# Kernel optimization log

Measured on AMD Instinct MI355X. Metric: run time of the kernel, lower is better.

## Reference

```python
import jax, jax.numpy as jnp
import numpy as np

HIDDEN = 64


def _lstm_cell(x, h, c, W_ih, W_hh, b_ih, b_hh):
    # gates: [B, 4*H], torch LSTMCell order: i, f, g, o
    gates = x @ W_ih.T + h @ W_hh.T + b_ih + b_hh
    i, f, g, o = jnp.split(gates, 4, axis=-1)
    i = jax.nn.sigmoid(i)
    f = jax.nn.sigmoid(f)
    g = jnp.tanh(g)
    o = jax.nn.sigmoid(o)
    c_new = f * c + i * g
    h_new = o * jnp.tanh(c_new)
    return h_new, c_new


def setup_inputs() -> dict:
    key = jax.random.key(0)
    ks = jax.random.split(key, 12)
    B, L, H = 1024, 512, HIDDEN
    k = 1.0 / np.sqrt(H)  # torch LSTMCell/Linear init scale
    u = lambda kk, shape: jax.random.uniform(kk, shape, jnp.float32, -k, k)
    return {
        "y": jax.random.normal(ks[0], (B, L), jnp.float32),
        "W_ih1": u(ks[1], (4 * H, 1)),
        "W_hh1": u(ks[2], (4 * H, H)),
        "b_ih1": u(ks[3], (4 * H,)),
        "b_hh1": u(ks[4], (4 * H,)),
        "W_ih2": u(ks[5], (4 * H, H)),
        "W_hh2": u(ks[6], (4 * H, H)),
        "b_ih2": u(ks[7], (4 * H,)),
        "b_hh2": u(ks[8], (4 * H,)),
        "W_lin": u(ks[9], (1, H)),
        "b_lin": u(ks[10], (1,)),
        "future_preds": 0,
    }


def reference(y, W_ih1, W_hh1, b_ih1, b_hh1, W_ih2, W_hh2, b_ih2, b_hh2,
              W_lin, b_lin, future_preds):
    B = y.shape[0]
    H = HIDDEN
    zeros = jnp.zeros((B, H), jnp.float32)

    def step(carry, x_t):
        h1, c1, h2, c2 = carry
        h1, c1 = _lstm_cell(x_t, h1, c1, W_ih1, W_hh1, b_ih1, b_hh1)
        h2, c2 = _lstm_cell(h1, h2, c2, W_ih2, W_hh2, b_ih2, b_hh2)
        out = h2 @ W_lin.T + b_lin  # [B, 1]
        return (h1, c1, h2, c2), out

    xs = y.T[:, :, None]  # [L, B, 1]
    carry, outs = jax.lax.scan(step, (zeros, zeros, zeros, zeros), xs)
    outputs = outs[:, :, 0].T  # [B, L]

    if future_preds > 0:
        def fstep(fc, _):
            h1, c1, h2, c2, out = fc
            h1, c1 = _lstm_cell(out, h1, c1, W_ih1, W_hh1, b_ih1, b_hh1)
            h2, c2 = _lstm_cell(h1, h2, c2, W_ih2, W_hh2, b_ih2, b_hh2)
            out = h2 @ W_lin.T + b_lin
            return (h1, c1, h2, c2, out), out
        last_out = outs[-1]  # [B, 1]
        _, fouts = jax.lax.scan(fstep, (*carry, last_out), None,
                                length=future_preds)
        outputs = jnp.concatenate([outputs, fouts[:, :, 0].T], axis=1)
    return outputs
```

## Files before the change

kernel.cpp:

```cpp
#include <hip/hip_runtime.h>
#include <math.h>

#define LSEQ 512

typedef float  f32x4  __attribute__((ext_vector_type(4)));
typedef short  bf16x8 __attribute__((ext_vector_type(8)));

union Frag { uint32_t u[4]; bf16x8 h; };

__device__ __forceinline__ float frcp(float x) { return __builtin_amdgcn_rcpf(x); }

__device__ __forceinline__ f32x4 vexp2(f32x4 x) {
    f32x4 r;
    r.x = exp2f(x.x); r.y = exp2f(x.y); r.z = exp2f(x.z); r.w = exp2f(x.w);
    return r;
}
__device__ __forceinline__ f32x4 vrcp(f32x4 x) {
    f32x4 r;
    r.x = frcp(x.x); r.y = frcp(x.y); r.z = frcp(x.z); r.w = frcp(x.w);
    return r;
}
__device__ __forceinline__ f32x4 vsigm(f32x4 x) {
    f32x4 e = vexp2(x * -1.442695041f);
    return vrcp(e + 1.0f);
}
__device__ __forceinline__ f32x4 vtanh(f32x4 x) {
    f32x4 e = vexp2(x * 2.885390082f);
    return 1.0f - 2.0f * vrcp(e + 1.0f);
}

__device__ __forceinline__ uint32_t pack_hi_u(uint32_t b0, uint32_t b1) {
    return __builtin_amdgcn_perm(b1, b0, 0x07060302u);
}

__device__ __forceinline__ void load_wfrag(const float* __restrict__ W, int sl, int nn, int g4,
                                           Frag fh[4][2], Frag fl[4][2]) {
#pragma unroll
    for (int gt = 0; gt < 4; ++gt) {
        const float* p = W + (size_t)(64 * gt + 16 * sl + nn) * 64 + g4 * 8;
#pragma unroll
        for (int kt = 0; kt < 2; ++kt) {
            float4 va = ((const float4*)(p + kt * 32))[0];
            float4 vb = ((const float4*)(p + kt * 32))[1];
            float v[8] = {va.x, va.y, va.z, va.w, vb.x, vb.y, vb.z, vb.w};
#pragma unroll
            for (int j = 0; j < 4; ++j) {
                uint32_t b0 = __float_as_uint(v[2 * j]);
                uint32_t b1 = __float_as_uint(v[2 * j + 1]);
                float l0 = v[2 * j]     - __uint_as_float(b0 & 0xffff0000u);
                float l1 = v[2 * j + 1] - __uint_as_float(b1 & 0xffff0000u);
                fh[gt][kt].u[j] = pack_hi_u(b0, b1);
                fl[gt][kt].u[j] = pack_hi_u(__float_as_uint(l0), __float_as_uint(l1));
            }
        }
    }
}

__device__ __forceinline__ int hidx(int m, int j) {
    return m * 64 + ((((j >> 3) ^ (m & 7)) << 3) | (j & 7));
}

__device__ __forceinline__ void loadA(const uint16_t* __restrict__ ph,
                                      const uint16_t* __restrict__ pl,
                                      int mm, int g4, bf16x8 ah[2], bf16x8 al[2]) {
#pragma unroll
    for (int kt = 0; kt < 2; ++kt) {
        const int off = mm * 64 + ((((kt << 2) + g4) ^ (mm & 7)) << 3);
        ah[kt] = *(const bf16x8*)(ph + off);
        al[kt] = *(const bf16x8*)(pl + off);
    }
}

__device__ __forceinline__ void split_store(uint16_t* ph, uint16_t* pl, int idx, float x) {
    uint32_t xb = __float_as_uint(x);
    ph[idx] = (uint16_t)(xb >> 16);
    float lo = x - __uint_as_float(xb & 0xffff0000u);
    pl[idx] = (uint16_t)(__float_as_uint(lo) >> 16);
}

#define MFMA3(acc, AH, AL, BH, BL)                                                  \
    acc = __builtin_amdgcn_mfma_f32_16x16x32_bf16((AH), (BH).h, acc, 0, 0, 0);      \
    acc = __builtin_amdgcn_mfma_f32_16x16x32_bf16((AH), (BL).h, acc, 0, 0, 0);      \
    acc = __builtin_amdgcn_mfma_f32_16x16x32_bf16((AL), (BH).h, acc, 0, 0, 0);

__global__ __launch_bounds__(512, 1)
void lstm2_pipe(const float* __restrict__ y,
                const float* __restrict__ W_ih1, const float* __restrict__ W_hh1,
                const float* __restrict__ b_ih1, const float* __restrict__ b_hh1,
                const float* __restrict__ W_ih2, const float* __restrict__ W_hh2,
                const float* __restrict__ b_ih2, const float* __restrict__ b_hh2,
                const float* __restrict__ W_lin, const float* __restrict__ b_lin,
                float* __restrict__ out)
{
    __shared__ __align__(16) float    y_s[LSEQ * 16];
    __shared__ __align__(16) uint16_t h1h[2][1024];
    __shared__ __align__(16) uint16_t h1l[2][1024];
    __shared__ __align__(16) uint16_t h2h[2][1024];
    __shared__ __align__(16) uint16_t h2l[2][1024];
    __shared__ __align__(16) float    outS[16 * 521];

    const int tid  = threadIdx.x;
    const int w    = tid >> 6;
    const int lane = tid & 63;
    const int nn   = lane & 15;
    const int g4   = lane >> 4;
    const int mq   = g4 << 2;
    const int bg0  = blockIdx.x << 4;

    {
        const int m = tid >> 5, seg = tid & 31;
        const float4* yp = (const float4*)(y + (size_t)(bg0 + m) * LSEQ) + seg * 4;
#pragma unroll
        for (int c = 0; c < 4; ++c) {
            float4 v = yp[c];
            int t0 = seg * 16 + c * 4;
            y_s[(t0 + 0) * 16 + m] = v.x;
            y_s[(t0 + 1) * 16 + m] = v.y;
            y_s[(t0 + 2) * 16 + m] = v.z;
            y_s[(t0 + 3) * 16 + m] = v.w;
        }
        if (tid < 256) {
            uint4 z = {0u, 0u, 0u, 0u};
            ((uint4*)h1h)[tid] = z;
            ((uint4*)h1l)[tid] = z;
            ((uint4*)h2h)[tid] = z;
            ((uint4*)h2l)[tid] = z;
        }
    }
    __syncthreads();

    if (w < 4) {
        Frag bh[4][2], bl[4][2];
        load_wfrag(W_hh1, w, nn, g4, bh, bl);
        float bs1_[4], wih1_[4];
#pragma unroll
        for (int gt = 0; gt < 4; ++gt) {
            int row = 64 * gt + 16 * w + nn;
            bs1_[gt]  = b_ih1[row] + b_hh1[row];
            wih1_[gt] = W_ih1[row];
        }
        const int jj = 16 * w + nn;
        f32x4 c1v = {0.f, 0.f, 0.f, 0.f};

        float wl[16];
        const float blin = b_lin[0];
        {
            const float4* wp = (const float4*)W_lin + g4 * 4;
#pragma unroll
            for (int i = 0; i < 4; ++i) {
                float4 v = wp[i];
                wl[4 * i + 0] = v.x; wl[4 * i + 1] = v.y;
                wl[4 * i + 2] = v.z; wl[4 * i + 3] = v.w;
            }
        }

#pragma unroll 1
        for (int t = 0; t <= LSEQ; ++t) {
            if (t < LSEQ) {
                bf16x8 ah[2], al[2];
                loadA(h1h[(t + 1) & 1], h1l[(t + 1) & 1], nn, g4, ah, al);
                f32x4 xq = *(const f32x4*)&y_s[t * 16 + mq];
                f32x4 ac0[4], ac1[4];
#pragma unroll
                for (int g = 0; g < 4; ++g) {
                    ac0[g] = xq * wih1_[g] + bs1_[g];
                    ac1[g] = 0.f;
                }
#pragma unroll
                for (int g = 0; g < 4; ++g) {
                    MFMA3(ac0[g], ah[0], al[0], bh[g][0], bl[g][0]);
                    MFMA3(ac1[g], ah[1], al[1], bh[g][1], bl[g][1]);
                }
                f32x4 gi = vsigm(ac0[0] + ac1[0]);
                f32x4 gf = vsigm(ac0[1] + ac1[1]);
                f32x4 gg = vtanh(ac0[2] + ac1[2]);
                f32x4 go = vsigm(ac0[3] + ac1[3]);
                c1v = gf * c1v + gi * gg;
                f32x4 h1v = go * vtanh(c1v);
#pragma unroll
                for (int r = 0; r < 4; ++r)
                    split_store(h1h[t & 1], h1l[t & 1], hidx(mq + r, jj), h1v[r]);
            }
            if (t >= 2 && w == ((t - 2) & 3)) {
                const uint16_t* ph = h2h[t & 1];
                const uint16_t* pl = h2l[t & 1];
                const int m = lane & 15;
                float s = 0.f;
#pragma unroll
                for (int oo = 0; oo < 2; ++oo) {
                    const int oct = 2 * g4 + oo;
                    const int off = m * 64 + ((oct ^ (m & 7)) << 3);
                    bf16x8 hv = *(const bf16x8*)(ph + off);
                    bf16x8 lv = *(const bf16x8*)(pl + off);
#pragma unroll
                    for (int i = 0; i < 8; ++i) {
                        float val = __uint_as_float(((uint32_t)(uint16_t)hv[i]) << 16)
                                  + __uint_as_float(((uint32_t)(uint16_t)lv[i]) << 16);
                        s = fmaf(val, wl[oo * 8 + i], s);
                    }
                }
                s += __shfl_xor(s, 16);
                s += __shfl_xor(s, 32);
                if (lane < 16) outS[m * 521 + (t - 2)] = s + blin;
            }
            __syncthreads();
        }
        if (w == 0) {
            const uint16_t* ph = h2h[1];
            const uint16_t* pl = h2l[1];
            const int m = lane & 15;
            float s = 0.f;
#pragma unroll
            for (int oo = 0; oo < 2; ++oo) {
                const int oct = 2 * g4 + oo;
                const int off = m * 64 + ((oct ^ (m & 7)) << 3);
                bf16x8 hv = *(const bf16x8*)(ph + off);
                bf16x8 lv = *(const bf16x8*)(pl + off);
#pragma unroll
                for (int i = 0; i < 8; ++i) {
                    float val = __uint_as_float(((uint32_t)(uint16_t)hv[i]) << 16)
                              + __uint_as_float(((uint32_t)(uint16_t)lv[i]) << 16);
                    s = fmaf(val, wl[oo * 8 + i], s);
                }
            }
            s += __shfl_xor(s, 16);
            s += __shfl_xor(s, 32);
            if (lane < 16) outS[m * 521 + (LSEQ - 1)] = s + blin;
        }
    } else {
        const int v = w - 4;
        Frag bih[4][2], bil[4][2], bhh[4][2], bhl[4][2];
        load_wfrag(W_ih2, v, nn, g4, bih, bil);
        load_wfrag(W_hh2, v, nn, g4, bhh, bhl);
        float bs2_[4];
#pragma unroll
        for (int gt = 0; gt < 4; ++gt) {
            int row = 64 * gt + 16 * v + nn;
            bs2_[gt] = b_ih2[row] + b_hh2[row];
        }
        const int jj = 16 * v + nn;
        f32x4 c2v = {0.f, 0.f, 0.f, 0.f};

#pragma unroll 1
        for (int t = 0; t <= LSEQ; ++t) {
            if (t >= 1) {
                bf16x8 a3h_[2], a3l_[2], a2h_[2], a2l_[2];
                loadA(h2h[t & 1],       h2l[t & 1],       nn, g4, a3h_, a3l_);
                loadA(h1h[(t - 1) & 1], h1l[(t - 1) & 1], nn, g4, a2h_, a2l_);
                f32x4 aca[4], acb[4];
#pragma unroll
                for (int g = 0; g < 4; ++g) { acb[g] = bs2_[g]; aca[g] = 0.f; }
                __builtin_amdgcn_s_setprio(1);
#pragma unroll
                for (int kt = 0; kt < 2; ++kt)
#pragma unroll
                    for (int g = 0; g < 4; ++g) {
                        MFMA3(acb[g], a3h_[kt], a3l_[kt], bhh[g][kt], bhl[g][kt]);
                        MFMA3(aca[g], a2h_[kt], a2l_[kt], bih[g][kt], bil[g][kt]);
                    }
                __builtin_amdgcn_s_setprio(0);
                f32x4 gi = vsigm(aca[0] + acb[0]);
                f32x4 gf = vsigm(aca[1] + acb[1]);
                f32x4 gg = vtanh(aca[2] + acb[2]);
                f32x4 go = vsigm(aca[3] + acb[3]);
                c2v = gf * c2v + gi * gg;
                f32x4 h2v = go * vtanh(c2v);
#pragma unroll
                for (int r = 0; r < 4; ++r)
                    split_store(h2h[(t - 1) & 1], h2l[(t - 1) & 1], hidx(mq + r, jj), h2v[r]);
            }
            __syncthreads();
        }
    }

    __syncthreads();

    {
        const int m  = tid >> 5;
        const int t0 = (tid & 31) << 4;
        float* op = out + (size_t)(bg0 + m) * LSEQ + t0;
        const float* sp = outS + m * 521 + t0;
#pragma unroll
        for (int k2 = 0; k2 < 4; ++k2) {
            float4 vv = make_float4(sp[4 * k2 + 0], sp[4 * k2 + 1],
                                    sp[4 * k2 + 2], sp[4 * k2 + 3]);
            *(float4*)(op + 4 * k2) = vv;
        }
    }
}

extern "C" void kernel_launch(void* const* d_in, const int* in_sizes, int n_in,
                              void* d_out, int out_size, void* d_ws, size_t ws_size,
                              hipStream_t stream) {
    const float* y     = (const float*)d_in[0];
    const float* W_ih1 = (const float*)d_in[1];
    const float* W_hh1 = (const float*)d_in[2];
    const float* b_ih1 = (const float*)d_in[3];
    const float* b_hh1 = (const float*)d_in[4];
    const float* W_ih2 = (const float*)d_in[5];
    const float* W_hh2 = (const float*)d_in[6];
    const float* b_ih2 = (const float*)d_in[7];
    const float* b_hh2 = (const float*)d_in[8];
    const float* W_lin = (const float*)d_in[9];
    const float* b_lin = (const float*)d_in[10];
    float* out = (float*)d_out;

    lstm2_pipe<<<dim3(64), dim3(512), 0, stream>>>(
        y, W_ih1, W_hh1, b_ih1, b_hh1, W_ih2, W_hh2, b_ih2, b_hh2,
        W_lin, b_lin, out);
}
```

Measured before the change: 826.6 us.

## Skew layer-2 input projection one step ahead and compute output head via MFMA

The layer-2 warps now compute the W_ih2·h1 projection one timestep ahead into a register accumulator, so each step's critical path only runs the W_hh2 recurrent MFMAs before the gate math. This lengthens the pipeline by one extra step. The scalar per-lane linear output head, which rotated across warps, is replaced by a single warp issuing MFMAs against a zero-padded W_lin fragment, with the outS layout transposed to match. Layer-1 MFMAs also get raised scheduling priority.

```diff
diff --git a/kernel.cpp b/kernel.cpp
--- a/kernel.cpp
+++ b/kernel.cpp
@@ -97,7 +97,7 @@
     __shared__ __align__(16) uint16_t h1l[2][1024];
     __shared__ __align__(16) uint16_t h2h[2][1024];
     __shared__ __align__(16) uint16_t h2l[2][1024];
-    __shared__ __align__(16) float    outS[16 * 521];
+    __shared__ __align__(16) float    outS[LSEQ * 20];
 
     const int tid  = threadIdx.x;
     const int w    = tid >> 6;
@@ -141,21 +141,33 @@
         }
         const int jj = 16 * w + nn;
         f32x4 c1v = {0.f, 0.f, 0.f, 0.f};
-
-        float wl[16];
         const float blin = b_lin[0];
-        {
-            const float4* wp = (const float4*)W_lin + g4 * 4;
-#pragma unroll
-            for (int i = 0; i < 4; ++i) {
-                float4 v = wp[i];
-                wl[4 * i + 0] = v.x; wl[4 * i + 1] = v.y;
-                wl[4 * i + 2] = v.z; wl[4 * i + 3] = v.w;
+
+        Frag wlh[2], wll[2];
+#pragma unroll
+        for (int kt = 0; kt < 2; ++kt) {
+            if (nn == 0) {
+                const float* p = W_lin + kt * 32 + g4 * 8;
+                float4 va = ((const float4*)p)[0];
+                float4 vb = ((const float4*)p)[1];
+                float vv[8] = {va.x, va.y, va.z, va.w, vb.x, vb.y, vb.z, vb.w};
+#pragma unroll
+                for (int j = 0; j < 4; ++j) {
+                    uint32_t b0 = __float_as_uint(vv[2 * j]);
+                    uint32_t b1 = __float_as_uint(vv[2 * j + 1]);
+                    float l0 = vv[2 * j]     - __uint_as_float(b0 & 0xffff0000u);
+                    float l1 = vv[2 * j + 1] - __uint_as_float(b1 & 0xffff0000u);
+                    wlh[kt].u[j] = pack_hi_u(b0, b1);
+                    wll[kt].u[j] = pack_hi_u(__float_as_uint(l0), __float_as_uint(l1));
+                }
+            } else {
+                wlh[kt].u[0] = wlh[kt].u[1] = wlh[kt].u[2] = wlh[kt].u[3] = 0u;
+                wll[kt].u[0] = wll[kt].u[1] = wll[kt].u[2] = wll[kt].u[3] = 0u;
             }
         }
 
 #pragma unroll 1
-        for (int t = 0; t <= LSEQ; ++t) {
+        for (int t = 0; t <= LSEQ + 1; ++t) {
             if (t < LSEQ) {
                 bf16x8 ah[2], al[2];
                 loadA(h1h[(t + 1) & 1], h1l[(t + 1) & 1], nn, g4, ah, al);
@@ -166,11 +178,13 @@
                     ac0[g] = xq * wih1_[g] + bs1_[g];
                     ac1[g] = 0.f;
                 }
+                __builtin_amdgcn_s_setprio(1);
 #pragma unroll
                 for (int g = 0; g < 4; ++g) {
                     MFMA3(ac0[g], ah[0], al[0], bh[g][0], bl[g][0]);
                     MFMA3(ac1[g], ah[1], al[1], bh[g][1], bl[g][1]);
                 }
+                __builtin_amdgcn_s_setprio(0);
                 f32x4 gi = vsigm(ac0[0] + ac1[0]);
                 f32x4 gf = vsigm(ac0[1] + ac1[1]);
                 f32x4 gg = vtanh(ac0[2] + ac1[2]);
@@ -181,51 +195,27 @@
                 for (int r = 0; r < 4; ++r)
                     split_store(h1h[t & 1], h1l[t & 1], hidx(mq + r, jj), h1v[r]);
             }
-            if (t >= 2 && w == ((t - 2) & 3)) {
-                const uint16_t* ph = h2h[t & 1];
-                const uint16_t* pl = h2l[t & 1];
-                const int m = lane & 15;
-                float s = 0.f;
-#pragma unroll
-                for (int oo = 0; oo < 2; ++oo) {
-                    const int oct = 2 * g4 + oo;
-                    const int off = m * 64 + ((oct ^ (m & 7)) << 3);
-                    bf16x8 hv = *(const bf16x8*)(ph + off);
-                    bf16x8 lv = *(const bf16x8*)(pl + off);
-#pragma unroll
-                    for (int i = 0; i < 8; ++i) {
-                        float val = __uint_as_float(((uint32_t)(uint16_t)hv[i]) << 16)
-                                  + __uint_as_float(((uint32_t)(uint16_t)lv[i]) << 16);
-                        s = fmaf(val, wl[oo * 8 + i], s);
-                    }
-                }
-                s += __shfl_xor(s, 16);
-                s += __shfl_xor(s, 32);
-                if (lane < 16) outS[m * 521 + (t - 2)] = s + blin;
+            if (w == 3 && t >= 3) {
+                bf16x8 a3h_[2], a3l_[2];
+                loadA(h2h[(t + 1) & 1], h2l[(t + 1) & 1], nn, g4, a3h_, a3l_);
+                f32x4 accD = {0.f, 0.f, 0.f, 0.f};
+                MFMA3(accD, a3h_[0], a3l_[0], wlh[0], wll[0]);
+                MFMA3(accD, a3h_[1], a3l_[1], wlh[1], wll[1]);
+                if (nn == 0) {
+                    *(f32x4*)&outS[(t - 3) * 20 + mq] = accD + blin;
+                }
             }
             __syncthreads();
         }
-        if (w == 0) {
-            const uint16_t* ph = h2h[1];
-            const uint16_t* pl = h2l[1];
-            const int m = lane & 15;
-            float s = 0.f;
-#pragma unroll
-            for (int oo = 0; oo < 2; ++oo) {
-                const int oct = 2 * g4 + oo;
-                const int off = m * 64 + ((oct ^ (m & 7)) << 3);
-                bf16x8 hv = *(const bf16x8*)(ph + off);
-                bf16x8 lv = *(const bf16x8*)(pl + off);
-#pragma unroll
-                for (int i = 0; i < 8; ++i) {
-                    float val = __uint_as_float(((uint32_t)(uint16_t)hv[i]) << 16)
-                              + __uint_as_float(((uint32_t)(uint16_t)lv[i]) << 16);
-                    s = fmaf(val, wl[oo * 8 + i], s);
-                }
-            }
-            s += __shfl_xor(s, 16);
-            s += __shfl_xor(s, 32);
-            if (lane < 16) outS[m * 521 + (LSEQ - 1)] = s + blin;
+        if (w == 3) {
+            bf16x8 a3h_[2], a3l_[2];
+            loadA(h2h[1], h2l[1], nn, g4, a3h_, a3l_);
+            f32x4 accD = {0.f, 0.f, 0.f, 0.f};
+            MFMA3(accD, a3h_[0], a3l_[0], wlh[0], wll[0]);
+            MFMA3(accD, a3h_[1], a3l_[1], wlh[1], wll[1]);
+            if (nn == 0) {
+                *(f32x4*)&outS[(LSEQ - 1) * 20 + mq] = accD + blin;
+            }
         }
     } else {
         const int v = w - 4;
@@ -240,34 +230,48 @@
         }
         const int jj = 16 * v + nn;
         f32x4 c2v = {0.f, 0.f, 0.f, 0.f};
+        f32x4 ihA[4];
+#pragma unroll
+        for (int g = 0; g < 4; ++g) ihA[g] = 0.f;
 
 #pragma unroll 1
-        for (int t = 0; t <= LSEQ; ++t) {
-            if (t >= 1) {
-                bf16x8 a3h_[2], a3l_[2], a2h_[2], a2l_[2];
-                loadA(h2h[t & 1],       h2l[t & 1],       nn, g4, a3h_, a3l_);
-                loadA(h1h[(t - 1) & 1], h1l[(t - 1) & 1], nn, g4, a2h_, a2l_);
-                f32x4 aca[4], acb[4];
-#pragma unroll
-                for (int g = 0; g < 4; ++g) { acb[g] = bs2_[g]; aca[g] = 0.f; }
+        for (int t = 0; t <= LSEQ + 1; ++t) {
+            if (t >= 2) {
+                bf16x8 a3h_[2], a3l_[2];
+                loadA(h2h[(t + 1) & 1], h2l[(t + 1) & 1], nn, g4, a3h_, a3l_);
+                f32x4 acb0[4], acb1[4];
+#pragma unroll
+                for (int g = 0; g < 4; ++g) { acb0[g] = 0.f; acb1[g] = 0.f; }
                 __builtin_amdgcn_s_setprio(1);
 #pragma unroll
-                for (int kt = 0; kt < 2; ++kt)
-#pragma unroll
-                    for (int g = 0; g < 4; ++g) {
-                        MFMA3(acb[g], a3h_[kt], a3l_[kt], bhh[g][kt], bhl[g][kt]);
-                        MFMA3(aca[g], a2h_[kt], a2l_[kt], bih[g][kt], bil[g][kt]);
-                    }
+                for (int g = 0; g < 4; ++g) {
+                    MFMA3(acb0[g], a3h_[0], a3l_[0], bhh[g][0], bhl[g][0]);
+                    MFMA3(acb1[g], a3h_[1], a3l_[1], bhh[g][1], bhl[g][1]);
+                }
                 __builtin_amdgcn_s_setprio(0);
-                f32x4 gi = vsigm(aca[0] + acb[0]);
-                f32x4 gf = vsigm(aca[1] + acb[1]);
-                f32x4 gg = vtanh(aca[2] + acb[2]);
-                f32x4 go = vsigm(aca[3] + acb[3]);
+                f32x4 gi = vsigm(ihA[0] + acb0[0] + acb1[0]);
+                f32x4 gf = vsigm(ihA[1] + acb0[1] + acb1[1]);
+                f32x4 gg = vtanh(ihA[2] + acb0[2] + acb1[2]);
+                f32x4 go = vsigm(ihA[3] + acb0[3] + acb1[3]);
                 c2v = gf * c2v + gi * gg;
                 f32x4 h2v = go * vtanh(c2v);
 #pragma unroll
                 for (int r = 0; r < 4; ++r)
-                    split_store(h2h[(t - 1) & 1], h2l[(t - 1) & 1], hidx(mq + r, jj), h2v[r]);
+                    split_store(h2h[t & 1], h2l[t & 1], hidx(mq + r, jj), h2v[r]);
+            }
+            if (t >= 1 && t <= LSEQ) {
+                bf16x8 a2h_[2], a2l_[2];
+                loadA(h1h[(t + 1) & 1], h1l[(t + 1) & 1], nn, g4, a2h_, a2l_);
+                f32x4 aca0[4], aca1[4];
+#pragma unroll
+                for (int g = 0; g < 4; ++g) { aca0[g] = bs2_[g]; aca1[g] = 0.f; }
+#pragma unroll
+                for (int g = 0; g < 4; ++g) {
+                    MFMA3(aca0[g], a2h_[0], a2l_[0], bih[g][0], bil[g][0]);
+                    MFMA3(aca1[g], a2h_[1], a2l_[1], bih[g][1], bil[g][1]);
+                }
+#pragma unroll
+                for (int g = 0; g < 4; ++g) ihA[g] = aca0[g] + aca1[g];
             }
             __syncthreads();
         }
@@ -279,11 +283,12 @@
         const int m  = tid >> 5;
         const int t0 = (tid & 31) << 4;
         float* op = out + (size_t)(bg0 + m) * LSEQ + t0;
-        const float* sp = outS + m * 521 + t0;
 #pragma unroll
         for (int k2 = 0; k2 < 4; ++k2) {
-            float4 vv = make_float4(sp[4 * k2 + 0], sp[4 * k2 + 1],
-                                    sp[4 * k2 + 2], sp[4 * k2 + 3]);
+            float4 vv = make_float4(outS[(t0 + 4 * k2 + 0) * 20 + m],
+                                    outS[(t0 + 4 * k2 + 1) * 20 + m],
+                                    outS[(t0 + 4 * k2 + 2) * 20 + m],
+                                    outS[(t0 + 4 * k2 + 3) * 20 + m]);
             *(float4*)(op + 4 * k2) = vv;
         }
     }
```

New measurement: 837.8 us. Within noise of the previous version (+1.4%).
